# Optimization experiments

Hardware: AMD Instinct MI355X
Metric: run time of the kernel (lower is better)

## Reference

```python
import jax, jax.numpy as jnp
import numpy as np

B, CIN, H, W = 32, 128, 64, 64
OUT, KH, KW = 256, 3, 3
NSK, SDIM = 4, 128


def setup_inputs() -> dict:
    key = jax.random.key(0)
    kx, kw_, kb, ks = jax.random.split(key, 4)
    x = jax.random.normal(kx, (B, CIN, H, W), dtype=jnp.float32)
    kval = float(np.sqrt(1.0 / (CIN * KH * KW)))  # groups=1
    weight = jax.random.uniform(kw_, (OUT, CIN, KH, KW), jnp.float32, -kval, kval)
    bias_tensor = jax.random.uniform(kb, (OUT,), jnp.float32, -kval, kval)
    # Rademacher / sketch_dim, shape (n, s, O) == torch's type1_signed_matrices
    signed = (2.0 * jax.random.bernoulli(ks, 0.5, (NSK, SDIM, OUT)).astype(jnp.float32) - 1.0) / SDIM
    # prod = einsum('ijkl,mi->mjkl') per sketch -> (n, s, Cin, kh, kw)
    prod = jnp.einsum('oikl,nso->nsikl', weight, signed)
    # .permute(2,3,1,0).flatten(0,2): (s,Cin,kh,kw) -> (kh,kw,Cin,s) -> (kh*kw*Cin, s)
    type1_sketches = prod.transpose(0, 3, 4, 2, 1).reshape(NSK, KH * KW * CIN, SDIM)
    return {
        "x": x,
        "type1_sketches": type1_sketches,
        "type1_signed_matrices": signed,
        "bias_tensor": bias_tensor,
    }


def reference(x, type1_sketches, type1_signed_matrices, bias_tensor):
    b, _, h1, w1 = x.shape
    h2 = h1 - KH + 1
    w2 = w1 - KW + 1
    # torch unfold: (B, Cin*KH*KW, E), features ordered channel-major (C, kh, kw)
    patches = jax.lax.conv_general_dilated_patches(
        x, filter_shape=(KH, KW), window_strides=(1, 1), padding='VALID'
    )  # (B, Cin*KH*KW, H2, W2)
    patches = patches.reshape(b, CIN * KH * KW, h2 * w2)  # (B, F, E)
    # 'bnfe,nfs->bnse' with the n-expansion folded away
    y = jnp.einsum('bfe,nfs->bnse', patches, type1_sketches)
    z = jnp.einsum('bnse,nso->bnoe', y, type1_signed_matrices)
    z = z.reshape(b, NSK, OUT, h2, w2)
    out = jnp.mean(z, axis=1) + bias_tensor[None, :, None, None]
    return out
```

## Files before the change

### kernel.cpp

```cpp
#include <hip/hip_runtime.h>
#include <hip/hip_bf16.h>
#include <stdint.h>


#define BATCH 32
#define CIN   128
#define HH    64
#define WW    64
#define OUTC  256
#define H2    62
#define W2    62
#define A_TILE 32768
#define WS_A_BYTES (18 * A_TILE)
#define BROWB 16384

typedef __bf16 bf16x8 __attribute__((ext_vector_type(8)));
typedef float  f32x4  __attribute__((ext_vector_type(4)));

typedef unsigned int u32_as1 __attribute__((address_space(1)));
typedef unsigned int u32_as3 __attribute__((address_space(3)));

__device__ __forceinline__ void async_copy16(const void* g, void* l) {
  __builtin_amdgcn_global_load_lds((const u32_as1*)g, (u32_as3*)l, 16, 0, 0);
}

#define FPB 4
__global__ __launch_bounds__(256) void weff_kernel(
    const float* __restrict__ sketches,
    const float* __restrict__ sgn,
    char* __restrict__ wsA)
{
  __shared__ alignas(16) float sk[512 * FPB];
  const int f0 = blockIdx.x * FPB;
  const int t  = threadIdx.x;

  for (int k = 0; k < (512 * FPB) / 256; ++k) {
    int idx = t + k * 256;
    int fi  = idx >> 9;
    int ns  = idx & 511;
    int n   = ns >> 7;
    int s   = ns & 127;
    sk[ns * FPB + fi] = sketches[(n * 1152 + f0 + fi) * 128 + s];
  }
  __syncthreads();

  const int o = t;
  float acc0 = 0.f, acc1 = 0.f, acc2 = 0.f, acc3 = 0.f;
#pragma unroll 8
  for (int ns = 0; ns < 512; ++ns) {
    float sg = sgn[ns * 256 + o];
    f32x4 skv = *(const f32x4*)(&sk[ns * FPB]);
    acc0 += sg * skv[0];
    acc1 += sg * skv[1];
    acc2 += sg * skv[2];
    acc3 += sg * skv[3];
  }

  float accs[FPB] = {acc0, acc1, acc2, acc3};
#pragma unroll
  for (int fi = 0; fi < FPB; ++fi) {
    int f    = f0 + fi;
    int c    = f / 9;
    int khkw = f - c * 9;
    int s    = khkw * 2 + (c >> 6);
    int kk   = c & 63;
    uint32_t byteoff = (uint32_t)s * A_TILE + (uint32_t)o * 128
                     + (((uint32_t)kk * 2u) ^ (uint32_t)((o & 7) << 4));
    *(__hip_bfloat16*)(wsA + byteoff) = __float2bfloat16(accs[fi] * 0.25f);
  }
}

__global__ __launch_bounds__(512, 2) void conv_kernel(
    const float* __restrict__ x,
    const char*  __restrict__ wA,
    const float* __restrict__ bias,
    float* __restrict__ out)
{
  __shared__ alignas(16) char lds[65536 + 6 * BROWB];
  char* ldsA = lds;
  char* ldsB = lds + 65536;

  const int bid = blockIdx.x;
  const int swz = (bid & 7) * 64 + (bid >> 3);
  const int b   = swz >> 4;
  const int ig  = swz & 15;
  const int i0  = ig * 4;

  const int t    = threadIdx.x;
  const int lane = t & 63;
  const int w    = t >> 6;
  const int wo   = w >> 2;
  const int we   = w & 3;

#define STAGE_A(LIN, BUF) do {                                             \
    const char* asrc_ = wA + (size_t)(LIN) * A_TILE + w * 1024 + lane * 16;\
    char* adst_ = ldsA + (BUF) * 32768 + w * 1024;                         \
    async_copy16(asrc_,          adst_);                                   \
    async_copy16(asrc_ + 8192,   adst_ + 8192);                            \
    async_copy16(asrc_ + 16384,  adst_ + 16384);                           \
    async_copy16(asrc_ + 24576,  adst_ + 24576);                           \
  } while (0)

  STAGE_A(0, 0);

  {
    const int j  = t & 63;
    const int cq = t >> 6;
    const uint32_t swb = (uint32_t)((j & 7) << 4);
#pragma unroll
    for (int r = 0; r < 6; ++r) {
      int xrow = i0 + r; if (xrow > 63) xrow = 63;
      const float* xr = x + (((size_t)(b * CIN + cq * 16)) * HH + xrow) * WW + j;
      char* lrow = ldsB + r * BROWB + j * 256;
#pragma unroll
      for (int g = 0; g < 2; ++g) {
        bf16x8 pk;
#pragma unroll
        for (int cc = 0; cc < 8; ++cc)
          pk[cc] = (__bf16)xr[(size_t)(g * 8 + cc) * (HH * WW)];
        uint32_t c0b = (uint32_t)(cq * 32 + g * 16);
        *(bf16x8*)(lrow + (c0b ^ swb)) = pk;
      }
    }
  }

  f32x4 acc[8][4];
  const f32x4 zf = {0.f, 0.f, 0.f, 0.f};
#pragma unroll
  for (int mi = 0; mi < 8; ++mi)
#pragma unroll
    for (int ni = 0; ni < 4; ++ni)
      acc[mi][ni] = zf;

  const int ln15  = lane & 15;
  const int khi16 = (lane >> 4) << 4;
  const uint32_t swa = (uint32_t)((ln15 & 7) << 4);
  const char* pAr = ldsA + (wo * 128 + ln15) * 128;
  const char* pA0 = pAr + (((uint32_t)khi16) ^ swa);
  const char* pA1 = pAr + (((uint32_t)(64 | khi16)) ^ swa);

#define MKB(COL, KS) (ldsB + (we * 64 + (COL)) * 256                       \
    + (((uint32_t)(((KS) << 6) | khi16)) ^ ((uint32_t)(((COL) & 7) << 4))))
  const char* pB00 = MKB(ln15 + 0, 0); const char* pB01 = MKB(ln15 + 0, 1);
  const char* pB10 = MKB(ln15 + 1, 0); const char* pB11 = MKB(ln15 + 1, 1);
  const char* pB20 = MKB(ln15 + 2, 0); const char* pB21 = MKB(ln15 + 2, 1);
  const int c30 = (48 + ln15 + 0 > 63) ? 63 : 48 + ln15 + 0;
  const int c31 = (48 + ln15 + 1 > 63) ? 63 : 48 + ln15 + 1;
  const int c32 = (48 + ln15 + 2 > 63) ? 63 : 48 + ln15 + 2;
  const char* pC00 = MKB(c30, 0); const char* pC01 = MKB(c30, 1);
  const char* pC10 = MKB(c31, 0); const char* pC11 = MKB(c31, 1);
  const char* pC20 = MKB(c32, 0); const char* pC21 = MKB(c32, 1);
#undef MKB

  __syncthreads();

#define MFMA_ __builtin_amdgcn_mfma_f32_16x16x32_bf16

#define KSH(AP, BP, CP, IMM, AIMM) do {                                    \
    bf16x8 b0_ = *(const bf16x8*)((BP) + (IMM));                           \
    bf16x8 b1_ = *(const bf16x8*)((BP) + (IMM) + 4096);                    \
    bf16x8 b2_ = *(const bf16x8*)((BP) + (IMM) + 8192);                    \
    bf16x8 b3_ = *(const bf16x8*)((CP) + (IMM));                           \
    bf16x8 a0_ = *(const bf16x8*)((AP) + (AIMM));                          \
    bf16x8 a1_ = *(const bf16x8*)((AP) + (AIMM) + 2048);                   \
    bf16x8 a2_ = *(const bf16x8*)((AP) + (AIMM) + 4096);                   \
    bf16x8 a3_ = *(const bf16x8*)((AP) + (AIMM) + 6144);                   \
    bf16x8 a4_ = *(const bf16x8*)((AP) + (AIMM) + 8192);                   \
    bf16x8 a5_ = *(const bf16x8*)((AP) + (AIMM) + 10240);                  \
    bf16x8 a6_ = *(const bf16x8*)((AP) + (AIMM) + 12288);                  \
    bf16x8 a7_ = *(const bf16x8*)((AP) + (AIMM) + 14336);                  \
    acc[0][0] = MFMA_(a0_, b0_, acc[0][0], 0, 0, 0);                       \
    acc[0][1] = MFMA_(a0_, b1_, acc[0][1], 0, 0, 0);                       \
    acc[0][2] = MFMA_(a0_, b2_, acc[0][2], 0, 0, 0);                       \
    acc[0][3] = MFMA_(a0_, b3_, acc[0][3], 0, 0, 0);                       \
    acc[1][0] = MFMA_(a1_, b0_, acc[1][0], 0, 0, 0);                       \
    acc[1][1] = MFMA_(a1_, b1_, acc[1][1], 0, 0, 0);                       \
    acc[1][2] = MFMA_(a1_, b2_, acc[1][2], 0, 0, 0);                       \
    acc[1][3] = MFMA_(a1_, b3_, acc[1][3], 0, 0, 0);                       \
    acc[2][0] = MFMA_(a2_, b0_, acc[2][0], 0, 0, 0);                       \
    acc[2][1] = MFMA_(a2_, b1_, acc[2][1], 0, 0, 0);                       \
    acc[2][2] = MFMA_(a2_, b2_, acc[2][2], 0, 0, 0);                       \
    acc[2][3] = MFMA_(a2_, b3_, acc[2][3], 0, 0, 0);                       \
    acc[3][0] = MFMA_(a3_, b0_, acc[3][0], 0, 0, 0);                       \
    acc[3][1] = MFMA_(a3_, b1_, acc[3][1], 0, 0, 0);                       \
    acc[3][2] = MFMA_(a3_, b2_, acc[3][2], 0, 0, 0);                       \
    acc[3][3] = MFMA_(a3_, b3_, acc[3][3], 0, 0, 0);                       \
    acc[4][0] = MFMA_(a4_, b0_, acc[4][0], 0, 0, 0);                       \
    acc[4][1] = MFMA_(a4_, b1_, acc[4][1], 0, 0, 0);                       \
    acc[4][2] = MFMA_(a4_, b2_, acc[4][2], 0, 0, 0);                       \
    acc[4][3] = MFMA_(a4_, b3_, acc[4][3], 0, 0, 0);                       \
    acc[5][0] = MFMA_(a5_, b0_, acc[5][0], 0, 0, 0);                       \
    acc[5][1] = MFMA_(a5_, b1_, acc[5][1], 0, 0, 0);                       \
    acc[5][2] = MFMA_(a5_, b2_, acc[5][2], 0, 0, 0);                       \
    acc[5][3] = MFMA_(a5_, b3_, acc[5][3], 0, 0, 0);                       \
    acc[6][0] = MFMA_(a6_, b0_, acc[6][0], 0, 0, 0);                       \
    acc[6][1] = MFMA_(a6_, b1_, acc[6][1], 0, 0, 0);                       \
    acc[6][2] = MFMA_(a6_, b2_, acc[6][2], 0, 0, 0);                       \
    acc[6][3] = MFMA_(a6_, b3_, acc[6][3], 0, 0, 0);                       \
    acc[7][0] = MFMA_(a7_, b0_, acc[7][0], 0, 0, 0);                       \
    acc[7][1] = MFMA_(a7_, b1_, acc[7][1], 0, 0, 0);                       \
    acc[7][2] = MFMA_(a7_, b2_, acc[7][2], 0, 0, 0);                       \
    acc[7][3] = MFMA_(a7_, b3_, acc[7][3], 0, 0, 0);                       \
  } while (0)

#define STEP(LIN, KH, KW) do {                                             \
    if ((LIN) < 17) STAGE_A((LIN) + 1, ((LIN) + 1) & 1);                   \
    KSH(pA0, pB##KW##0, pC##KW##0,                                         \
        (KH) * BROWB + ((LIN) & 1) * 128, ((LIN) & 1) * 32768);            \
    KSH(pA1, pB##KW##1, pC##KW##1,                                         \
        (KH) * BROWB + ((LIN) & 1) * 128, ((LIN) & 1) * 32768);            \
    if ((LIN) < 17) __syncthreads();                                       \
  } while (0)

  STEP(0, 0, 0);   STEP(1, 0, 0);
  STEP(2, 0, 1);   STEP(3, 0, 1);
  STEP(4, 0, 2);   STEP(5, 0, 2);
  STEP(6, 1, 0);   STEP(7, 1, 0);
  STEP(8, 1, 1);   STEP(9, 1, 1);
  STEP(10, 1, 2);  STEP(11, 1, 2);
  STEP(12, 2, 0);  STEP(13, 2, 0);
  STEP(14, 2, 1);  STEP(15, 2, 1);
  STEP(16, 2, 2);  STEP(17, 2, 2);

#undef STEP
#undef KSH
#undef MFMA_
#undef STAGE_A

  const int jn   = ln15;
  const int g4   = lane >> 4;
  const int irow = i0 + we;
  if (irow < H2) {
#pragma unroll
    for (int mi = 0; mi < 8; ++mi) {
#pragma unroll
      for (int ni = 0; ni < 4; ++ni) {
        const int jj = (ni << 4) + jn;
        if (jj < W2) {
#pragma unroll
          for (int rr = 0; rr < 4; ++rr) {
            const int o = (wo << 7) + (mi << 4) + (g4 << 2) + rr;
            out[(((size_t)b * OUTC + o) * H2 + irow) * W2 + jj] =
                acc[mi][ni][rr] + bias[o];
          }
        }
      }
    }
  }
}

extern "C" void kernel_launch(void* const* d_in, const int* in_sizes, int n_in,
                              void* d_out, int out_size, void* d_ws, size_t ws_size,
                              hipStream_t stream) {
  const float* x        = (const float*)d_in[0];
  const float* sketches = (const float*)d_in[1];
  const float* sgn      = (const float*)d_in[2];
  const float* bias     = (const float*)d_in[3];
  float* out            = (float*)d_out;
  char* wsA             = (char*)d_ws;

  if (ws_size < (size_t)WS_A_BYTES) return;

  weff_kernel<<<1152 / FPB, 256, 0, stream>>>(sketches, sgn, wsA);
  conv_kernel<<<BATCH * 16, 512, 0, stream>>>(x, wsA, bias, out);
}
```

Baseline: 106.5 us.

## Triple-buffer smaller A tiles with vmcnt-based waits and MFMA priority

```diff
diff --git a/kernel.cpp b/kernel.cpp
--- a/kernel.cpp
+++ b/kernel.cpp
@@ -10,8 +10,8 @@
 #define OUTC  256
 #define H2    62
 #define W2    62
-#define A_TILE 32768
-#define WS_A_BYTES (18 * A_TILE)
+#define A_TILE 16384
+#define WS_A_BYTES (36 * A_TILE)
 #define BROWB 16384
 
 typedef __bf16 bf16x8 __attribute__((ext_vector_type(8)));
@@ -62,10 +62,11 @@
     int f    = f0 + fi;
     int c    = f / 9;
     int khkw = f - c * 9;
-    int s    = khkw * 2 + (c >> 6);
-    int kk   = c & 63;
-    uint32_t byteoff = (uint32_t)s * A_TILE + (uint32_t)o * 128
-                     + (((uint32_t)kk * 2u) ^ (uint32_t)((o & 7) << 4));
+    int st   = khkw * 4 + (c >> 5);
+    int kk   = c & 31;
+    uint32_t byteoff = (uint32_t)st * A_TILE + (uint32_t)o * 64
+                     + (((uint32_t)kk * 2u) ^ (uint32_t)((o & 3) << 4)
+                                            ^ (uint32_t)((o & 4) << 2));
     *(__hip_bfloat16*)(wsA + byteoff) = __float2bfloat16(accs[fi] * 0.25f);
   }
 }
@@ -76,9 +77,9 @@
     const float* __restrict__ bias,
     float* __restrict__ out)
 {
-  __shared__ alignas(16) char lds[65536 + 6 * BROWB];
+  __shared__ alignas(16) char lds[3 * A_TILE + 6 * BROWB];
   char* ldsA = lds;
-  char* ldsB = lds + 65536;
+  char* ldsB = lds + 3 * A_TILE;
 
   const int bid = blockIdx.x;
   const int swz = (bid & 7) * 64 + (bid >> 3);
@@ -92,16 +93,15 @@
   const int wo   = w >> 2;
   const int we   = w & 3;
 
-#define STAGE_A(LIN, BUF) do {                                             \
-    const char* asrc_ = wA + (size_t)(LIN) * A_TILE + w * 1024 + lane * 16;\
-    char* adst_ = ldsA + (BUF) * 32768 + w * 1024;                         \
-    async_copy16(asrc_,          adst_);                                   \
-    async_copy16(asrc_ + 8192,   adst_ + 8192);                            \
-    async_copy16(asrc_ + 16384,  adst_ + 16384);                           \
-    async_copy16(asrc_ + 24576,  adst_ + 24576);                           \
+#define STAGE_A(ST, BUF) do {                                              \
+    const char* asrc_ = wA + (size_t)(ST) * A_TILE + w * 2048 + lane * 16; \
+    char* adst_ = ldsA + (BUF) * A_TILE + w * 2048;                        \
+    async_copy16(asrc_,         adst_);                                    \
+    async_copy16(asrc_ + 1024,  adst_ + 1024);                             \
   } while (0)
 
   STAGE_A(0, 0);
+  STAGE_A(1, 1);
 
   {
     const int j  = t & 63;
@@ -134,41 +134,49 @@
 
   const int ln15  = lane & 15;
   const int khi16 = (lane >> 4) << 4;
-  const uint32_t swa = (uint32_t)((ln15 & 7) << 4);
-  const char* pAr = ldsA + (wo * 128 + ln15) * 128;
-  const char* pA0 = pAr + (((uint32_t)khi16) ^ swa);
-  const char* pA1 = pAr + (((uint32_t)(64 | khi16)) ^ swa);
-
-#define MKB(COL, KS) (ldsB + (we * 64 + (COL)) * 256                       \
-    + (((uint32_t)(((KS) << 6) | khi16)) ^ ((uint32_t)(((COL) & 7) << 4))))
-  const char* pB00 = MKB(ln15 + 0, 0); const char* pB01 = MKB(ln15 + 0, 1);
-  const char* pB10 = MKB(ln15 + 1, 0); const char* pB11 = MKB(ln15 + 1, 1);
-  const char* pB20 = MKB(ln15 + 2, 0); const char* pB21 = MKB(ln15 + 2, 1);
+  const char* pA = ldsA + (wo * 128 + ln15) * 64
+                 + (((uint32_t)khi16) ^ ((uint32_t)((ln15 & 3) << 4))
+                                      ^ ((uint32_t)((ln15 & 4) << 2)));
+
+#define MKB(COL, PAR) (ldsB + we * BROWB + (COL) * 256                     \
+    + (((uint32_t)khi16) ^ ((uint32_t)(((COL) & 3) << 4)))                 \
+    + (uint32_t)((((PAR) ^ (((COL) >> 2) & 1)) & 1) * 64))
+  const char* pB0E = MKB(ln15 + 0, 0); const char* pB0O = MKB(ln15 + 0, 1);
+  const char* pB1E = MKB(ln15 + 1, 0); const char* pB1O = MKB(ln15 + 1, 1);
+  const char* pB2E = MKB(ln15 + 2, 0); const char* pB2O = MKB(ln15 + 2, 1);
   const int c30 = (48 + ln15 + 0 > 63) ? 63 : 48 + ln15 + 0;
   const int c31 = (48 + ln15 + 1 > 63) ? 63 : 48 + ln15 + 1;
   const int c32 = (48 + ln15 + 2 > 63) ? 63 : 48 + ln15 + 2;
-  const char* pC00 = MKB(c30, 0); const char* pC01 = MKB(c30, 1);
-  const char* pC10 = MKB(c31, 0); const char* pC11 = MKB(c31, 1);
-  const char* pC20 = MKB(c32, 0); const char* pC21 = MKB(c32, 1);
+  const char* pC0E = MKB(c30, 0); const char* pC0O = MKB(c30, 1);
+  const char* pC1E = MKB(c31, 0); const char* pC1O = MKB(c31, 1);
+  const char* pC2E = MKB(c32, 0); const char* pC2O = MKB(c32, 1);
 #undef MKB
 
-  __syncthreads();
+  asm volatile("s_waitcnt lgkmcnt(0)" ::: "memory");
 
 #define MFMA_ __builtin_amdgcn_mfma_f32_16x16x32_bf16
-
-#define KSH(AP, BP, CP, IMM, AIMM) do {                                    \
-    bf16x8 b0_ = *(const bf16x8*)((BP) + (IMM));                           \
-    bf16x8 b1_ = *(const bf16x8*)((BP) + (IMM) + 4096);                    \
-    bf16x8 b2_ = *(const bf16x8*)((BP) + (IMM) + 8192);                    \
-    bf16x8 b3_ = *(const bf16x8*)((CP) + (IMM));                           \
-    bf16x8 a0_ = *(const bf16x8*)((AP) + (AIMM));                          \
-    bf16x8 a1_ = *(const bf16x8*)((AP) + (AIMM) + 2048);                   \
-    bf16x8 a2_ = *(const bf16x8*)((AP) + (AIMM) + 4096);                   \
-    bf16x8 a3_ = *(const bf16x8*)((AP) + (AIMM) + 6144);                   \
-    bf16x8 a4_ = *(const bf16x8*)((AP) + (AIMM) + 8192);                   \
-    bf16x8 a5_ = *(const bf16x8*)((AP) + (AIMM) + 10240);                  \
-    bf16x8 a6_ = *(const bf16x8*)((AP) + (AIMM) + 12288);                  \
-    bf16x8 a7_ = *(const bf16x8*)((AP) + (AIMM) + 14336);                  \
+#define WVM2 asm volatile("s_waitcnt vmcnt(2)" ::: "memory")
+#define WVM0 asm volatile("s_waitcnt vmcnt(0)" ::: "memory")
+
+#define STEP(ST, KH, KW, CSH, PAR, BUF, TGT, WVM) do {                     \
+    WVM;                                                                   \
+    __builtin_amdgcn_s_barrier();                                          \
+    if ((ST) < 34) STAGE_A((ST) + 2, TGT);                                 \
+    const int bimm_ = (KH) * BROWB + (CSH) * 128;                          \
+    const int aimm_ = (BUF) * A_TILE;                                      \
+    bf16x8 b0_ = *(const bf16x8*)(pB##KW##PAR + bimm_);                    \
+    bf16x8 b1_ = *(const bf16x8*)(pB##KW##PAR + bimm_ + 4096);             \
+    bf16x8 b2_ = *(const bf16x8*)(pB##KW##PAR + bimm_ + 8192);             \
+    bf16x8 b3_ = *(const bf16x8*)(pC##KW##PAR + bimm_);                    \
+    bf16x8 a0_ = *(const bf16x8*)(pA + aimm_);                             \
+    bf16x8 a1_ = *(const bf16x8*)(pA + aimm_ + 1024);                      \
+    bf16x8 a2_ = *(const bf16x8*)(pA + aimm_ + 2048);                      \
+    bf16x8 a3_ = *(const bf16x8*)(pA + aimm_ + 3072);                      \
+    bf16x8 a4_ = *(const bf16x8*)(pA + aimm_ + 4096);                      \
+    bf16x8 a5_ = *(const bf16x8*)(pA + aimm_ + 5120);                      \
+    bf16x8 a6_ = *(const bf16x8*)(pA + aimm_ + 6144);                      \
+    bf16x8 a7_ = *(const bf16x8*)(pA + aimm_ + 7168);                      \
+    __builtin_amdgcn_s_setprio(1);                                         \
     acc[0][0] = MFMA_(a0_, b0_, acc[0][0], 0, 0, 0);                       \
     acc[0][1] = MFMA_(a0_, b1_, acc[0][1], 0, 0, 0);                       \
     acc[0][2] = MFMA_(a0_, b2_, acc[0][2], 0, 0, 0);                       \
@@ -201,29 +209,31 @@
     acc[7][1] = MFMA_(a7_, b1_, acc[7][1], 0, 0, 0);                       \
     acc[7][2] = MFMA_(a7_, b2_, acc[7][2], 0, 0, 0);                       \
     acc[7][3] = MFMA_(a7_, b3_, acc[7][3], 0, 0, 0);                       \
+    __builtin_amdgcn_s_setprio(0);                                         \
   } while (0)
 
-#define STEP(LIN, KH, KW) do {                                             \
-    if ((LIN) < 17) STAGE_A((LIN) + 1, ((LIN) + 1) & 1);                   \
-    KSH(pA0, pB##KW##0, pC##KW##0,                                         \
-        (KH) * BROWB + ((LIN) & 1) * 128, ((LIN) & 1) * 32768);            \
-    KSH(pA1, pB##KW##1, pC##KW##1,                                         \
-        (KH) * BROWB + ((LIN) & 1) * 128, ((LIN) & 1) * 32768);            \
-    if ((LIN) < 17) __syncthreads();                                       \
-  } while (0)
-
-  STEP(0, 0, 0);   STEP(1, 0, 0);
-  STEP(2, 0, 1);   STEP(3, 0, 1);
-  STEP(4, 0, 2);   STEP(5, 0, 2);
-  STEP(6, 1, 0);   STEP(7, 1, 0);
-  STEP(8, 1, 1);   STEP(9, 1, 1);
-  STEP(10, 1, 2);  STEP(11, 1, 2);
-  STEP(12, 2, 0);  STEP(13, 2, 0);
-  STEP(14, 2, 1);  STEP(15, 2, 1);
-  STEP(16, 2, 2);  STEP(17, 2, 2);
+  STEP(0,  0,0, 0,E, 0, 2, WVM2);  STEP(1,  0,0, 0,O, 1, 0, WVM2);
+  STEP(2,  0,0, 1,E, 2, 1, WVM2);  STEP(3,  0,0, 1,O, 0, 2, WVM2);
+  STEP(4,  0,1, 0,E, 1, 0, WVM2);  STEP(5,  0,1, 0,O, 2, 1, WVM2);
+  STEP(6,  0,1, 1,E, 0, 2, WVM2);  STEP(7,  0,1, 1,O, 1, 0, WVM2);
+  STEP(8,  0,2, 0,E, 2, 1, WVM2);  STEP(9,  0,2, 0,O, 0, 2, WVM2);
+  STEP(10, 0,2, 1,E, 1, 0, WVM2);  STEP(11, 0,2, 1,O, 2, 1, WVM2);
+  STEP(12, 1,0, 0,E, 0, 2, WVM2);  STEP(13, 1,0, 0,O, 1, 0, WVM2);
+  STEP(14, 1,0, 1,E, 2, 1, WVM2);  STEP(15, 1,0, 1,O, 0, 2, WVM2);
+  STEP(16, 1,1, 0,E, 1, 0, WVM2);  STEP(17, 1,1, 0,O, 2, 1, WVM2);
+  STEP(18, 1,1, 1,E, 0, 2, WVM2);  STEP(19, 1,1, 1,O, 1, 0, WVM2);
+  STEP(20, 1,2, 0,E, 2, 1, WVM2);  STEP(21, 1,2, 0,O, 0, 2, WVM2);
+  STEP(22, 1,2, 1,E, 1, 0, WVM2);  STEP(23, 1,2, 1,O, 2, 1, WVM2);
+  STEP(24, 2,0, 0,E, 0, 2, WVM2);  STEP(25, 2,0, 0,O, 1, 0, WVM2);
+  STEP(26, 2,0, 1,E, 2, 1, WVM2);  STEP(27, 2,0, 1,O, 0, 2, WVM2);
+  STEP(28, 2,1, 0,E, 1, 0, WVM2);  STEP(29, 2,1, 0,O, 2, 1, WVM2);
+  STEP(30, 2,1, 1,E, 0, 2, WVM2);  STEP(31, 2,1, 1,O, 1, 0, WVM2);
+  STEP(32, 2,2, 0,E, 2, 1, WVM2);  STEP(33, 2,2, 0,O, 0, 2, WVM2);
+  STEP(34, 2,2, 1,E, 1, 0, WVM2);  STEP(35, 2,2, 1,O, 2, 1, WVM0);
 
 #undef STEP
-#undef KSH
+#undef WVM0
+#undef WVM2
 #undef MFMA_
 #undef STAGE_A
 
```

Measured after the change: 110.0 us. +3.2%, slower.
